# Kernel tuning notes

Hardware: AMD Instinct MI355X
Metric: run time of the kernel (lower is better)

Reference implementation:

```python
import jax, jax.numpy as jnp
import numpy as np

B, C, H, W = 8, 32, 120, 160
MAX_ITER = 3
DAMP = 1e-4
OCC_THRES = 0.1

def setup_inputs():
    key = jax.random.key(0)
    ks = jax.random.split(key, 7)
    R = jnp.broadcast_to(jnp.eye(3, dtype=jnp.float32), (B, 3, 3))
    t = 0.01 * jax.random.normal(ks[0], (B, 3), jnp.float32)
    F0 = jax.random.normal(ks[1], (B, C, H, W), jnp.float32)
    F1 = jax.random.normal(ks[2], (B, C, H, W), jnp.float32)
    invD0 = 0.1 + 0.9 * jax.random.uniform(ks[3], (B, 1, H, W), dtype=jnp.float32)
    invD1 = 0.1 + 0.9 * jax.random.uniform(ks[4], (B, 1, H, W), dtype=jnp.float32)
    K = jnp.broadcast_to(jnp.array([150.0, 150.0, (W - 1) / 2.0, (H - 1) / 2.0], jnp.float32), (B, 4))
    sigma0 = jax.random.uniform(ks[5], (B, 1, H, W), dtype=jnp.float32)
    sigma1 = jax.random.uniform(ks[6], (B, 1, H, W), dtype=jnp.float32)
    return {"R": R, "t": t, "F0": F0, "F1": F1, "invD0": invD0, "invD1": invD1,
            "K": K, "sigma0": sigma0, "sigma1": sigma1}

def _sobel_grad(F):
    # Sobel gradient with replicate padding, normalized (feature_gradient)
    b, c, h, w = F.shape
    kx = jnp.array([[-1., 0., 1.], [-2., 0., 2.], [-1., 0., 1.]], F.dtype).reshape(1, 1, 3, 3)
    ky = jnp.array([[-1., -2., -1.], [0., 0., 0.], [1., 2., 1.]], F.dtype).reshape(1, 1, 3, 3)
    Fp = jnp.pad(F.reshape(b * c, 1, h, w), ((0, 0), (0, 0), (1, 1), (1, 1)), mode='edge')
    dn = ('NCHW', 'OIHW', 'NCHW')
    dx = jax.lax.conv_general_dilated(Fp, kx, (1, 1), 'VALID', dimension_numbers=dn)
    dy = jax.lax.conv_general_dilated(Fp, ky, (1, 1), 'VALID', dimension_numbers=dn)
    mag = jnp.sqrt(dx * dx + dy * dy + 1e-8)
    return (dx / mag).reshape(b, c, h, w), (dy / mag).reshape(b, c, h, w)

def _warp_features(F, u, v):
    # bilinear sampling of F [B,C,H,W] at pixel coords u, v [B,1,H,W], border clamp
    b, c, h, w = F.shape
    u = jnp.clip(u.reshape(b, -1), 0.0, w - 1.0)
    v = jnp.clip(v.reshape(b, -1), 0.0, h - 1.0)
    x0 = jnp.floor(u); y0 = jnp.floor(v)
    wx = (u - x0)[:, None, :]; wy = (v - y0)[:, None, :]
    x0i = x0.astype(jnp.int32); y0i = y0.astype(jnp.int32)
    x1i = jnp.minimum(x0i + 1, w - 1); y1i = jnp.minimum(y0i + 1, h - 1)
    Ff = F.reshape(b, c, h * w)
    def g(yi, xi):
        idx = jnp.broadcast_to((yi * w + xi)[:, None, :], (b, c, yi.shape[-1]))
        return jnp.take_along_axis(Ff, idx, axis=2)
    out = (g(y0i, x0i) * (1 - wx) * (1 - wy) + g(y0i, x1i) * wx * (1 - wy)
           + g(y1i, x0i) * (1 - wx) * wy + g(y1i, x1i) * wx * wy)
    return out.reshape(b, c, h, w)

def _xy_grid(K, b, h, w):
    fx, fy, cx, cy = K[:, 0], K[:, 1], K[:, 2], K[:, 3]
    uu, vv = jnp.meshgrid(jnp.arange(w, dtype=K.dtype), jnp.arange(h, dtype=K.dtype))
    px = (uu[None] - cx[:, None, None]) / fx[:, None, None]
    py = (vv[None] - cy[:, None, None]) / fy[:, None, None]
    return px[:, None], py[:, None]  # [B,1,H,W]

def _warp_inverse_depth(px, py, invD, Rm, t, K):
    b, _, h, w = px.shape
    xyz = jnp.concatenate([px, py, jnp.ones_like(px)], axis=1).reshape(b, 3, h * w)
    warped = jnp.matmul(Rm, xyz) + t[:, :, None] * invD.reshape(b, 1, h * w)
    x_, y_, s_ = warped[:, 0], warped[:, 1], warped[:, 2]
    fx, fy, cx, cy = K[:, 0:1], K[:, 1:2], K[:, 2:3], K[:, 3:4]
    u = (x_ / s_) * fx + cx
    v = (y_ / s_) * fy + cy
    inv_z = invD.reshape(b, h * w) / s_
    return u.reshape(b, 1, h, w), v.reshape(b, 1, h, w), inv_z.reshape(b, 1, h, w)

def _jacobian_warping(invD, K, px, py, Rm, t):
    # compute_Jacobian_warping with pose: returns dx_dp, dy_dp each [B,HW,6]
    b, _, h, w = invD.shape
    xyz = jnp.concatenate([px, py, invD], axis=1).reshape(b, 3, h * w)
    warped = jnp.matmul(Rm, xyz) + t[:, :, None]
    x = warped[:, 0][..., None]; y = warped[:, 1][..., None]; iz = warped[:, 2][..., None]
    xy = x * y
    o = jnp.zeros_like(x)
    dx_dp = jnp.concatenate([-xy, 1 + x * x, -y, iz, o, -iz * x], axis=2)
    dy_dp = jnp.concatenate([-1 - y * y, xy, x, o, iz, -iz * y], axis=2)
    fx = K[:, 0].reshape(b, 1, 1); fy = K[:, 1].reshape(b, 1, 1)
    return dx_dp * fx, dy_dp * fy

def _se3_exp(xi):
    # xi [B,6] = [omega(3), v(3)] matching Jacobian column order (rotation first)
    w = xi[:, :3]; v = xi[:, 3:]
    th2 = jnp.sum(w * w, axis=1, keepdims=True)
    th = jnp.sqrt(th2 + 1e-12)
    a = jnp.sin(th) / th
    bb = (1 - jnp.cos(th)) / (th2 + 1e-12)
    cc = (1 - a) / (th2 + 1e-12)
    z = jnp.zeros_like(w[:, 0])
    wx = jnp.stack([z, -w[:, 2], w[:, 1],
                    w[:, 2], z, -w[:, 0],
                    -w[:, 1], w[:, 0], z], axis=1).reshape(-1, 3, 3)
    wx2 = jnp.matmul(wx, wx)
    I = jnp.eye(3, dtype=xi.dtype)[None]
    Rm = I + a[..., None] * wx + bb[..., None] * wx2
    V = I + bb[..., None] * wx + cc[..., None] * wx2
    dt = jnp.matmul(V, v[..., None])[..., 0]
    return Rm, dt

def _forward(R, t, F0, F1, invD0, invD1, K, sigma0, sigma1):
    b, c, h, w = F0.shape
    hw = h * w
    px, py = _xy_grid(K, b, h, w)
    # feature gradient of F1 is pose-independent -> hoisted out of the loop
    JF_x, JF_y = _sobel_grad(F1)
    weights = jnp.ones_like(F0)
    for _ in range(MAX_ITER):
        # --- compute_warped_residual ---
        u, v, inv_z = _warp_inverse_depth(px, py, invD0, R, t, K)
        F1w = _warp_features(F1, u, v)
        invD1w = _warp_features(invD1, u, v)
        inview = (u > 0) & (u < w - 1) & (v > 0) & (v < h - 1)
        occ = ~((inv_z > invD1w - OCC_THRES) & inview)  # [B,1,H,W]
        res = jnp.where(occ, jnp.asarray(0.001, F0.dtype), F1w - F0)  # [B,C,H,W]
        # --- compute_Jacobian (J_p = -dF/dp) ---
        JFxw = _warp_features(JF_x, u, v).reshape(b, c, hw, 1)
        JFyw = _warp_features(JF_y, u, v).reshape(b, c, hw, 1)
        Jx_p, Jy_p = _jacobian_warping(invD0, K, px, py, R, t)  # [B,HW,6]
        J_p = -(JFxw * Jx_p[:, None] + JFyw * Jy_p[:, None]).reshape(b, c * hw, 6)
        # --- robust weights (Cauchy m-estimator stand-in for mEst_func) ---
        weights = 1.0 / (1.0 + res * res)
        # --- damped Gauss-Newton solve (directSolver stand-in) ---
        JtWJ = jnp.einsum('bnk,bnl->bkl', J_p, J_p)
        rhs = jnp.einsum('bnk,bn->bk', J_p, (weights * res).reshape(b, -1))
        A = JtWJ + DAMP * jnp.eye(6, dtype=J_p.dtype)[None]
        dp = jnp.linalg.solve(A, rhs[..., None])[..., 0]
        dR, dt = _se3_exp(dp)
        t = jnp.matmul(dR, t[..., None])[..., 0] + dt
        R = jnp.matmul(dR, R)
    # pack pose + weights into one array: [B, 9 + 3 + C*H*W]
    return jnp.concatenate([R.reshape(b, 9), t, weights.reshape(b, -1)], axis=1)

def reference(R, t, F0, F1, invD0, invD1, K, sigma0, sigma1):
    return _forward(R, t, F0, F1, invD0, invD1, K, sigma0, sigma1)
```

## Files before the change

### kernel.cpp

```cpp
#include <hip/hip_runtime.h>
#include <math.h>

#define Bn 8
#define Cn 32
#define Hn 120
#define Wn 160
#define HW (Hn*Wn)
#define CHW (Cn*HW)
#define OUTB (12 + CHW)
#define DAMP_C 1e-4
#define OCC_THRES_C 0.1f

#define NCG 4
#define CPG (Cn/NCG)
#define BPB (HW/256)

__global__ void init_kernel(const float* __restrict__ R_in,
                            const float* __restrict__ t_in,
                            float* __restrict__ pose,
                            float* __restrict__ accum) {
    int b = threadIdx.x;
    if (b < Bn) {
        for (int i = 0; i < 9; ++i) pose[b*12 + i] = R_in[b*9 + i];
        for (int i = 0; i < 3; ++i) pose[b*12 + 9 + i] = t_in[b*3 + i];
        for (int i = 0; i < 32; ++i) accum[b*32 + i] = 0.0f;
    }
}

__global__ __launch_bounds__(256) void sobel_kernel(const float* __restrict__ F1,
                                                    float2* __restrict__ G) {
    int idx = blockIdx.x * 256 + threadIdx.x;
    int p = idx % HW;
    int plane = idx / HW;
    int y = p / Wn, x = p % Wn;
    const float* Fp = F1 + (size_t)plane * HW;
    int ym = max(y-1, 0) * Wn, yc = y * Wn, yp = min(y+1, Hn-1) * Wn;
    int xm = max(x-1, 0), xp = min(x+1, Wn-1);
    float a00 = Fp[ym+xm], a01 = Fp[ym+x], a02 = Fp[ym+xp];
    float a10 = Fp[yc+xm],                 a12 = Fp[yc+xp];
    float a20 = Fp[yp+xm], a21 = Fp[yp+x], a22 = Fp[yp+xp];
    float dx = (a02 - a00) + 2.0f*(a12 - a10) + (a22 - a20);
    float dy = (a20 - a00) + 2.0f*(a21 - a01) + (a22 - a02);
    float mag = sqrtf(dx*dx + dy*dy + 1e-8f);
    G[idx] = make_float2(dx / mag, dy / mag);
}

template<bool LAST>
__global__ __launch_bounds__(256) void accum_kernel(
    const float* __restrict__ F0, const float* __restrict__ F1,
    const float* __restrict__ invD0, const float* __restrict__ invD1,
    const float* __restrict__ Kin,
    const float2* __restrict__ G,
    const float* __restrict__ pose, float* __restrict__ accum,
    float* __restrict__ out)
{
    __shared__ float sp[16];
    __shared__ float sred[4*27];
    int blk = blockIdx.x;
    int pblk = blk % BPB;
    int cg   = (blk / BPB) % NCG;
    int b    = blk / (BPB * NCG);
    int p = pblk * 256 + threadIdx.x;
    if (threadIdx.x < 12) sp[threadIdx.x] = pose[b*12 + threadIdx.x];
    else if (threadIdx.x < 16) sp[threadIdx.x] = Kin[b*4 + threadIdx.x - 12];
    __syncthreads();
    float R0=sp[0],R1=sp[1],R2=sp[2],R3=sp[3],R4=sp[4],R5=sp[5],R6=sp[6],R7=sp[7],R8=sp[8];
    float t0=sp[9],t1=sp[10],t2=sp[11];
    float fx=sp[12],fy=sp[13],cx=sp[14],cy=sp[15];

    int y = p / Wn, x = p % Wn;
    float px = ((float)x - cx) / fx;
    float py = ((float)y - cy) / fy;
    float d = invD0[(size_t)b*HW + p];

    float X = R0*px + R1*py + R2 + t0*d;
    float Y = R3*px + R4*py + R5 + t1*d;
    float S = R6*px + R7*py + R8 + t2*d;
    float u = X / S * fx + cx;
    float v = Y / S * fy + cy;
    float iz = d / S;
    bool inview = (u > 0.0f) && (u < (float)(Wn-1)) && (v > 0.0f) && (v < (float)(Hn-1));

    float uc = fminf(fmaxf(u, 0.0f), (float)(Wn-1));
    float vc = fminf(fmaxf(v, 0.0f), (float)(Hn-1));
    float x0f = floorf(uc), y0f = floorf(vc);
    float wx = uc - x0f, wy = vc - y0f;
    int x0 = (int)x0f, y0 = (int)y0f;
    int x1 = min(x0+1, Wn-1), y1 = min(y0+1, Hn-1);
    int i00 = y0*Wn + x0, i01 = y0*Wn + x1, i10 = y1*Wn + x0, i11 = y1*Wn + x1;
    float w00 = (1.0f-wx)*(1.0f-wy), w01 = wx*(1.0f-wy);
    float w10 = (1.0f-wx)*wy,        w11 = wx*wy;

    const float* iD1 = invD1 + (size_t)b*HW;
    float invD1w = iD1[i00]*w00 + iD1[i01]*w01 + iD1[i10]*w10 + iD1[i11]*w11;
    bool occ = !((iz > invD1w - OCC_THRES_C) && inview);

    float xj  = R0*px + R1*py + R2*d + t0;
    float yj  = R3*px + R4*py + R5*d + t1;
    float izj = R6*px + R7*py + R8*d + t2;
    float Jx[6], Jy[6];
    Jx[0] = -xj*yj*fx;        Jx[1] = (1.0f + xj*xj)*fx; Jx[2] = -yj*fx;
    Jx[3] = izj*fx;           Jx[4] = 0.0f;              Jx[5] = -izj*xj*fx;
    Jy[0] = -(1.0f + yj*yj)*fy; Jy[1] = xj*yj*fy;        Jy[2] = xj*fy;
    Jy[3] = 0.0f;             Jy[4] = izj*fy;            Jy[5] = -izj*yj*fy;

    const float*  F0b = F0 + (size_t)b*CHW + p;
    const float*  F1b = F1 + (size_t)b*CHW;
    const float2* Gb  = G  + (size_t)b*CHW;
    int cbase0 = cg * CPG * HW;
    float A2 = 0.0f, B2 = 0.0f, ABc = 0.0f, Sx = 0.0f, Sy = 0.0f;
    #pragma unroll
    for (int cc = 0; cc < CPG; ++cc) {
        int base = cbase0 + cc * HW;
        float2 g00 = Gb[base+i00], g01 = Gb[base+i01];
        float2 g10 = Gb[base+i10], g11 = Gb[base+i11];
        float f1w = F1b[base+i00]*w00 + F1b[base+i01]*w01 + F1b[base+i10]*w10 + F1b[base+i11]*w11;
        float gx  = g00.x*w00 + g01.x*w01 + g10.x*w10 + g11.x*w11;
        float gy  = g00.y*w00 + g01.y*w01 + g10.y*w10 + g11.y*w11;
        float r = occ ? 0.001f : (f1w - F0b[base]);
        float wt = 1.0f / (1.0f + r*r);
        if (LAST) __builtin_nontemporal_store(wt, &out[(size_t)b*OUTB + 12 + base + p]);
        A2 += gx*gx; B2 += gy*gy; ABc += gx*gy;
        float wr = wt * r;
        Sx += wr*gx; Sy += wr*gy;
    }

    float part[27];
    {
        int idx = 0;
        #pragma unroll
        for (int k = 0; k < 6; ++k)
            #pragma unroll
            for (int l = k; l < 6; ++l)
                part[idx++] = A2*Jx[k]*Jx[l] + ABc*(Jx[k]*Jy[l] + Jy[k]*Jx[l]) + B2*Jy[k]*Jy[l];
        #pragma unroll
        for (int k = 0; k < 6; ++k) part[21+k] = -(Sx*Jx[k] + Sy*Jy[k]);
    }

    #pragma unroll
    for (int i = 0; i < 27; ++i) {
        float vsum = part[i];
        for (int off = 32; off > 0; off >>= 1) vsum += __shfl_down(vsum, off, 64);
        part[i] = vsum;
    }
    int lane = threadIdx.x & 63, wave = threadIdx.x >> 6;
    if (lane == 0)
        for (int i = 0; i < 27; ++i) sred[wave*27 + i] = part[i];
    __syncthreads();
    if (threadIdx.x < 27) {
        float s = sred[threadIdx.x] + sred[27+threadIdx.x] + sred[54+threadIdx.x] + sred[81+threadIdx.x];
        atomicAdd(&accum[b*32 + threadIdx.x], s);
    }
}

__global__ void solve_kernel(float* __restrict__ pose, float* __restrict__ accum,
                             float* __restrict__ out, int write_out) {
    int b = threadIdx.x;
    if (b >= Bn) return;
    double A[6][7];
    {
        float acc[27];
        for (int i = 0; i < 27; ++i) acc[i] = accum[b*32 + i];
        int idx = 0;
        for (int k = 0; k < 6; ++k)
            for (int l = k; l < 6; ++l) {
                double vv = (double)acc[idx++];
                A[k][l] = vv; A[l][k] = vv;
            }
        for (int k = 0; k < 6; ++k) { A[k][k] += DAMP_C; A[k][6] = (double)acc[21+k]; }
        for (int i = 0; i < 32; ++i) accum[b*32 + i] = 0.0f;
    }
    for (int col = 0; col < 6; ++col) {
        int piv = col;
        double mx = fabs(A[col][col]);
        for (int r = col+1; r < 6; ++r) { double a = fabs(A[r][col]); if (a > mx) { mx = a; piv = r; } }
        if (piv != col)
            for (int j = col; j < 7; ++j) { double tmp = A[col][j]; A[col][j] = A[piv][j]; A[piv][j] = tmp; }
        double inv = 1.0 / A[col][col];
        for (int r = col+1; r < 6; ++r) {
            double f = A[r][col] * inv;
            for (int j = col; j < 7; ++j) A[r][j] -= f * A[col][j];
        }
    }
    double dp[6];
    for (int col = 5; col >= 0; --col) {
        double s = A[col][6];
        for (int j = col+1; j < 6; ++j) s -= A[col][j] * dp[j];
        dp[col] = s / A[col][col];
    }
    double w0 = dp[0], w1 = dp[1], w2 = dp[2];
    double v0 = dp[3], v1 = dp[4], v2 = dp[5];
    double th2 = w0*w0 + w1*w1 + w2*w2;
    double th = sqrt(th2 + 1e-12);
    float thf = (float)th;
    double sth = (double)sinf(thf);
    double cth = (double)cosf(thf);
    double a = sth / th;
    double bb = (1.0 - cth) / (th2 + 1e-12);
    double cc = (1.0 - a) / (th2 + 1e-12);
    double wxm[3][3] = {{0,-w2,w1},{w2,0,-w0},{-w1,w0,0}};
    double wx2[3][3];
    for (int i = 0; i < 3; ++i)
        for (int j = 0; j < 3; ++j) {
            double s = 0;
            for (int k = 0; k < 3; ++k) s += wxm[i][k]*wxm[k][j];
            wx2[i][j] = s;
        }
    double dR[3][3], V[3][3];
    for (int i = 0; i < 3; ++i)
        for (int j = 0; j < 3; ++j) {
            double I = (i == j) ? 1.0 : 0.0;
            dR[i][j] = I + a*wxm[i][j] + bb*wx2[i][j];
            V[i][j]  = I + bb*wxm[i][j] + cc*wx2[i][j];
        }
    double dt[3];
    for (int i = 0; i < 3; ++i) dt[i] = V[i][0]*v0 + V[i][1]*v1 + V[i][2]*v2;
    double Ro[3][3], to[3];
    for (int i = 0; i < 9; ++i) Ro[i/3][i%3] = (double)pose[b*12 + i];
    for (int i = 0; i < 3; ++i) to[i] = (double)pose[b*12 + 9 + i];
    double tn[3], Rn[3][3];
    for (int i = 0; i < 3; ++i)
        tn[i] = dR[i][0]*to[0] + dR[i][1]*to[1] + dR[i][2]*to[2] + dt[i];
    for (int i = 0; i < 3; ++i)
        for (int j = 0; j < 3; ++j)
            Rn[i][j] = dR[i][0]*Ro[0][j] + dR[i][1]*Ro[1][j] + dR[i][2]*Ro[2][j];
    for (int i = 0; i < 9; ++i) pose[b*12 + i] = (float)Rn[i/3][i%3];
    for (int i = 0; i < 3; ++i) pose[b*12 + 9 + i] = (float)tn[i];
    if (write_out) {
        for (int i = 0; i < 9; ++i) out[(size_t)b*OUTB + i] = (float)Rn[i/3][i%3];
        for (int i = 0; i < 3; ++i) out[(size_t)b*OUTB + 9 + i] = (float)tn[i];
    }
}

extern "C" void kernel_launch(void* const* d_in, const int* in_sizes, int n_in,
                              void* d_out, int out_size, void* d_ws, size_t ws_size,
                              hipStream_t stream) {
    const float* R_in  = (const float*)d_in[0];
    const float* t_in  = (const float*)d_in[1];
    const float* F0    = (const float*)d_in[2];
    const float* F1    = (const float*)d_in[3];
    const float* invD0 = (const float*)d_in[4];
    const float* invD1 = (const float*)d_in[5];
    const float* Kin   = (const float*)d_in[6];
    float* out = (float*)d_out;

    float2* G    = (float2*)d_ws;
    float* accum = (float*)(G + (size_t)Bn*CHW);
    float* pose  = accum + Bn*32;

    init_kernel<<<1, 64, 0, stream>>>(R_in, t_in, pose, accum);
    sobel_kernel<<<(Bn*CHW)/256, 256, 0, stream>>>(F1, G);

    for (int it = 0; it < 3; ++it) {
        bool last = (it == 2);
        if (last)
            accum_kernel<true><<<Bn*NCG*BPB, 256, 0, stream>>>(
                F0, F1, invD0, invD1, Kin, G, pose, accum, out);
        else
            accum_kernel<false><<<Bn*NCG*BPB, 256, 0, stream>>>(
                F0, F1, invD0, invD1, Kin, G, pose, accum, out);
        solve_kernel<<<1, 64, 0, stream>>>(pose, accum, out, last ? 1 : 0);
    }
}
```

Measured before the change: 250.2 us.

## Store gradients and features in fp16 and batch gather loads per channel group

The prep kernel now writes the Sobel gradients, F1 and F0 as half precision copies, and the accumulation kernel reads these instead of the fp32 tensors. The gather loop is split into two groups of four channels, with all loads issued before the arithmetic to expose memory-level parallelism. This cuts the bytes read in each of the three Gauss-Newton iterations, at the cost of an extra conversion pass over F0 and F1. It also adds fp16 rounding error to the residuals and weights, which may exceed the output tolerance.

```diff
diff --git a/kernel.cpp b/kernel.cpp
--- a/kernel.cpp
+++ b/kernel.cpp
@@ -1,4 +1,5 @@
 #include <hip/hip_runtime.h>
+#include <hip/hip_fp16.h>
 #include <math.h>
 
 #define Bn 8
@@ -27,8 +28,11 @@
     }
 }
 
-__global__ __launch_bounds__(256) void sobel_kernel(const float* __restrict__ F1,
-                                                    float2* __restrict__ G) {
+__global__ __launch_bounds__(256) void prep_kernel(const float* __restrict__ F1,
+                                                   const float* __restrict__ F0,
+                                                   __half2* __restrict__ Gh,
+                                                   __half* __restrict__ F1h,
+                                                   __half* __restrict__ F0h) {
     int idx = blockIdx.x * 256 + threadIdx.x;
     int p = idx % HW;
     int plane = idx / HW;
@@ -37,20 +41,22 @@
     int ym = max(y-1, 0) * Wn, yc = y * Wn, yp = min(y+1, Hn-1) * Wn;
     int xm = max(x-1, 0), xp = min(x+1, Wn-1);
     float a00 = Fp[ym+xm], a01 = Fp[ym+x], a02 = Fp[ym+xp];
-    float a10 = Fp[yc+xm],                 a12 = Fp[yc+xp];
+    float a10 = Fp[yc+xm], a11 = Fp[yc+x], a12 = Fp[yc+xp];
     float a20 = Fp[yp+xm], a21 = Fp[yp+x], a22 = Fp[yp+xp];
     float dx = (a02 - a00) + 2.0f*(a12 - a10) + (a22 - a20);
     float dy = (a20 - a00) + 2.0f*(a21 - a01) + (a22 - a02);
     float mag = sqrtf(dx*dx + dy*dy + 1e-8f);
-    G[idx] = make_float2(dx / mag, dy / mag);
+    Gh[idx]  = __floats2half2_rn(dx / mag, dy / mag);
+    F1h[idx] = __float2half(a11);
+    F0h[idx] = __float2half(F0[idx]);
 }
 
 template<bool LAST>
 __global__ __launch_bounds__(256) void accum_kernel(
-    const float* __restrict__ F0, const float* __restrict__ F1,
     const float* __restrict__ invD0, const float* __restrict__ invD1,
     const float* __restrict__ Kin,
-    const float2* __restrict__ G,
+    const __half* __restrict__ F1h, const __half* __restrict__ F0h,
+    const __half2* __restrict__ Gh,
     const float* __restrict__ pose, float* __restrict__ accum,
     float* __restrict__ out)
 {
@@ -104,25 +110,40 @@
     Jy[0] = -(1.0f + yj*yj)*fy; Jy[1] = xj*yj*fy;        Jy[2] = xj*fy;
     Jy[3] = 0.0f;             Jy[4] = izj*fy;            Jy[5] = -izj*yj*fy;
 
-    const float*  F0b = F0 + (size_t)b*CHW + p;
-    const float*  F1b = F1 + (size_t)b*CHW;
-    const float2* Gb  = G  + (size_t)b*CHW;
+    const __half*  F1b = F1h + (size_t)b*CHW;
+    const __half*  F0b = F0h + (size_t)b*CHW + p;
+    const __half2* Gb  = Gh  + (size_t)b*CHW;
     int cbase0 = cg * CPG * HW;
     float A2 = 0.0f, B2 = 0.0f, ABc = 0.0f, Sx = 0.0f, Sy = 0.0f;
     #pragma unroll
-    for (int cc = 0; cc < CPG; ++cc) {
-        int base = cbase0 + cc * HW;
-        float2 g00 = Gb[base+i00], g01 = Gb[base+i01];
-        float2 g10 = Gb[base+i10], g11 = Gb[base+i11];
-        float f1w = F1b[base+i00]*w00 + F1b[base+i01]*w01 + F1b[base+i10]*w10 + F1b[base+i11]*w11;
-        float gx  = g00.x*w00 + g01.x*w01 + g10.x*w10 + g11.x*w11;
-        float gy  = g00.y*w00 + g01.y*w01 + g10.y*w10 + g11.y*w11;
-        float r = occ ? 0.001f : (f1w - F0b[base]);
-        float wt = 1.0f / (1.0f + r*r);
-        if (LAST) __builtin_nontemporal_store(wt, &out[(size_t)b*OUTB + 12 + base + p]);
-        A2 += gx*gx; B2 += gy*gy; ABc += gx*gy;
-        float wr = wt * r;
-        Sx += wr*gx; Sy += wr*gy;
+    for (int hb = 0; hb < 2; ++hb) {
+        __half  l00[4], l01[4], l10[4], l11[4], lf0[4];
+        __half2 g00[4], g01[4], g10[4], g11[4];
+        #pragma unroll
+        for (int cc = 0; cc < 4; ++cc) {
+            int base = cbase0 + (hb*4 + cc) * HW;
+            l00[cc] = F1b[base+i00]; l01[cc] = F1b[base+i01];
+            l10[cc] = F1b[base+i10]; l11[cc] = F1b[base+i11];
+            g00[cc] = Gb[base+i00];  g01[cc] = Gb[base+i01];
+            g10[cc] = Gb[base+i10];  g11[cc] = Gb[base+i11];
+            lf0[cc] = F0b[base];
+        }
+        #pragma unroll
+        for (int cc = 0; cc < 4; ++cc) {
+            int base = cbase0 + (hb*4 + cc) * HW;
+            float f1w = __half2float(l00[cc])*w00 + __half2float(l01[cc])*w01
+                      + __half2float(l10[cc])*w10 + __half2float(l11[cc])*w11;
+            float2 G00 = __half22float2(g00[cc]), G01 = __half22float2(g01[cc]);
+            float2 G10 = __half22float2(g10[cc]), G11 = __half22float2(g11[cc]);
+            float gx = G00.x*w00 + G01.x*w01 + G10.x*w10 + G11.x*w11;
+            float gy = G00.y*w00 + G01.y*w01 + G10.y*w10 + G11.y*w11;
+            float r = occ ? 0.001f : (f1w - __half2float(lf0[cc]));
+            float wt = 1.0f / (1.0f + r*r);
+            if (LAST) __builtin_nontemporal_store(wt, &out[(size_t)b*OUTB + 12 + base + p]);
+            A2 += gx*gx; B2 += gy*gy; ABc += gx*gy;
+            float wr = wt * r;
+            Sx += wr*gx; Sy += wr*gy;
+        }
     }
 
     float part[27];
@@ -244,21 +265,23 @@
     const float* Kin   = (const float*)d_in[6];
     float* out = (float*)d_out;
 
-    float2* G    = (float2*)d_ws;
-    float* accum = (float*)(G + (size_t)Bn*CHW);
+    __half2* Gh  = (__half2*)d_ws;
+    __half*  F1h = (__half*)(Gh + (size_t)Bn*CHW);
+    __half*  F0h = F1h + (size_t)Bn*CHW;
+    float* accum = (float*)(F0h + (size_t)Bn*CHW);
     float* pose  = accum + Bn*32;
 
     init_kernel<<<1, 64, 0, stream>>>(R_in, t_in, pose, accum);
-    sobel_kernel<<<(Bn*CHW)/256, 256, 0, stream>>>(F1, G);
+    prep_kernel<<<(Bn*CHW)/256, 256, 0, stream>>>(F1, F0, Gh, F1h, F0h);
 
     for (int it = 0; it < 3; ++it) {
         bool last = (it == 2);
         if (last)
             accum_kernel<true><<<Bn*NCG*BPB, 256, 0, stream>>>(
-                F0, F1, invD0, invD1, Kin, G, pose, accum, out);
+                invD0, invD1, Kin, F1h, F0h, Gh, pose, accum, out);
         else
             accum_kernel<false><<<Bn*NCG*BPB, 256, 0, stream>>>(
-                F0, F1, invD0, invD1, Kin, G, pose, accum, out);
+                invD0, invD1, Kin, F1h, F0h, Gh, pose, accum, out);
         solve_kernel<<<1, 64, 0, stream>>>(pose, accum, out, last ? 1 : 0);
     }
 }
```

After: 228.2 us. -8.8%, faster.

## Store features and gradients as channel-last fp16 for vectorized bilinear gathers

Applied to the files above, without the earlier changes.

The prep kernel now writes Sobel gradients, F1 and F0 in a pixel-major, channel-innermost layout using half precision. The accumulation kernel then fetches each channel group's eight values per bilinear corner with a few 16-byte loads instead of many scattered fp32 loads. This cuts gather traffic and the number of memory transactions across the three Gauss-Newton iterations. The cost is fp16 rounding of features and gradients, which changes numerics, plus a strided transposed write pattern in the prep kernel.

```diff
diff --git a/kernel.cpp b/kernel.cpp
--- a/kernel.cpp
+++ b/kernel.cpp
@@ -1,4 +1,5 @@
 #include <hip/hip_runtime.h>
+#include <hip/hip_fp16.h>
 #include <math.h>
 
 #define Bn 8
@@ -15,6 +16,9 @@
 #define CPG (Cn/NCG)
 #define BPB (HW/256)
 
+union H8  { ulonglong2 q;    __half  h[8];  };
+union G8  { ulonglong2 q[2]; __half2 h2[8]; };
+
 __global__ void init_kernel(const float* __restrict__ R_in,
                             const float* __restrict__ t_in,
                             float* __restrict__ pose,
@@ -27,30 +31,37 @@
     }
 }
 
-__global__ __launch_bounds__(256) void sobel_kernel(const float* __restrict__ F1,
-                                                    float2* __restrict__ G) {
+__global__ __launch_bounds__(256) void prep_kernel(const float* __restrict__ F1,
+                                                   const float* __restrict__ F0,
+                                                   __half2* __restrict__ Gt,
+                                                   __half* __restrict__ F1t,
+                                                   __half* __restrict__ F0t) {
     int idx = blockIdx.x * 256 + threadIdx.x;
     int p = idx % HW;
     int plane = idx / HW;
+    int b = plane / Cn, c = plane % Cn;
     int y = p / Wn, x = p % Wn;
     const float* Fp = F1 + (size_t)plane * HW;
     int ym = max(y-1, 0) * Wn, yc = y * Wn, yp = min(y+1, Hn-1) * Wn;
     int xm = max(x-1, 0), xp = min(x+1, Wn-1);
     float a00 = Fp[ym+xm], a01 = Fp[ym+x], a02 = Fp[ym+xp];
-    float a10 = Fp[yc+xm],                 a12 = Fp[yc+xp];
+    float a10 = Fp[yc+xm], a11 = Fp[yc+x], a12 = Fp[yc+xp];
     float a20 = Fp[yp+xm], a21 = Fp[yp+x], a22 = Fp[yp+xp];
     float dx = (a02 - a00) + 2.0f*(a12 - a10) + (a22 - a20);
     float dy = (a20 - a00) + 2.0f*(a21 - a01) + (a22 - a02);
     float mag = sqrtf(dx*dx + dy*dy + 1e-8f);
-    G[idx] = make_float2(dx / mag, dy / mag);
+    size_t tidx = ((size_t)b*HW + p)*Cn + c;
+    Gt[tidx]  = __floats2half2_rn(dx / mag, dy / mag);
+    F1t[tidx] = __float2half(a11);
+    F0t[tidx] = __float2half(F0[idx]);
 }
 
 template<bool LAST>
 __global__ __launch_bounds__(256) void accum_kernel(
-    const float* __restrict__ F0, const float* __restrict__ F1,
     const float* __restrict__ invD0, const float* __restrict__ invD1,
     const float* __restrict__ Kin,
-    const float2* __restrict__ G,
+    const __half* __restrict__ F1t, const __half* __restrict__ F0t,
+    const __half2* __restrict__ Gt,
     const float* __restrict__ pose, float* __restrict__ accum,
     float* __restrict__ out)
 {
@@ -104,22 +115,40 @@
     Jy[0] = -(1.0f + yj*yj)*fy; Jy[1] = xj*yj*fy;        Jy[2] = xj*fy;
     Jy[3] = 0.0f;             Jy[4] = izj*fy;            Jy[5] = -izj*yj*fy;
 
-    const float*  F0b = F0 + (size_t)b*CHW + p;
-    const float*  F1b = F1 + (size_t)b*CHW;
-    const float2* Gb  = G  + (size_t)b*CHW;
-    int cbase0 = cg * CPG * HW;
+    const __half*  F1b = F1t + (size_t)b*HW*Cn;
+    const __half*  F0b = F0t + (size_t)b*HW*Cn;
+    const __half2* Gb  = Gt  + (size_t)b*HW*Cn;
+    int co = cg * CPG;
+    size_t t00 = (size_t)i00*Cn + co, t01 = (size_t)i01*Cn + co;
+    size_t t10 = (size_t)i10*Cn + co, t11 = (size_t)i11*Cn + co;
+    H8 f00, f01, f10, f11, ff0;
+    G8 g00, g01, g10, g11;
+    f00.q = *reinterpret_cast<const ulonglong2*>(F1b + t00);
+    f01.q = *reinterpret_cast<const ulonglong2*>(F1b + t01);
+    f10.q = *reinterpret_cast<const ulonglong2*>(F1b + t10);
+    f11.q = *reinterpret_cast<const ulonglong2*>(F1b + t11);
+    g00.q[0] = *reinterpret_cast<const ulonglong2*>(Gb + t00);
+    g00.q[1] = *reinterpret_cast<const ulonglong2*>(Gb + t00 + 4);
+    g01.q[0] = *reinterpret_cast<const ulonglong2*>(Gb + t01);
+    g01.q[1] = *reinterpret_cast<const ulonglong2*>(Gb + t01 + 4);
+    g10.q[0] = *reinterpret_cast<const ulonglong2*>(Gb + t10);
+    g10.q[1] = *reinterpret_cast<const ulonglong2*>(Gb + t10 + 4);
+    g11.q[0] = *reinterpret_cast<const ulonglong2*>(Gb + t11);
+    g11.q[1] = *reinterpret_cast<const ulonglong2*>(Gb + t11 + 4);
+    ff0.q = *reinterpret_cast<const ulonglong2*>(F0b + (size_t)p*Cn + co);
+
     float A2 = 0.0f, B2 = 0.0f, ABc = 0.0f, Sx = 0.0f, Sy = 0.0f;
     #pragma unroll
     for (int cc = 0; cc < CPG; ++cc) {
-        int base = cbase0 + cc * HW;
-        float2 g00 = Gb[base+i00], g01 = Gb[base+i01];
-        float2 g10 = Gb[base+i10], g11 = Gb[base+i11];
-        float f1w = F1b[base+i00]*w00 + F1b[base+i01]*w01 + F1b[base+i10]*w10 + F1b[base+i11]*w11;
-        float gx  = g00.x*w00 + g01.x*w01 + g10.x*w10 + g11.x*w11;
-        float gy  = g00.y*w00 + g01.y*w01 + g10.y*w10 + g11.y*w11;
-        float r = occ ? 0.001f : (f1w - F0b[base]);
+        float f1w = __half2float(f00.h[cc])*w00 + __half2float(f01.h[cc])*w01
+                  + __half2float(f10.h[cc])*w10 + __half2float(f11.h[cc])*w11;
+        float2 G00 = __half22float2(g00.h2[cc]), G01 = __half22float2(g01.h2[cc]);
+        float2 G10 = __half22float2(g10.h2[cc]), G11 = __half22float2(g11.h2[cc]);
+        float gx = G00.x*w00 + G01.x*w01 + G10.x*w10 + G11.x*w11;
+        float gy = G00.y*w00 + G01.y*w01 + G10.y*w10 + G11.y*w11;
+        float r = occ ? 0.001f : (f1w - __half2float(ff0.h[cc]));
         float wt = 1.0f / (1.0f + r*r);
-        if (LAST) __builtin_nontemporal_store(wt, &out[(size_t)b*OUTB + 12 + base + p]);
+        if (LAST) __builtin_nontemporal_store(wt, &out[(size_t)b*OUTB + 12 + (co+cc)*HW + p]);
         A2 += gx*gx; B2 += gy*gy; ABc += gx*gy;
         float wr = wt * r;
         Sx += wr*gx; Sy += wr*gy;
@@ -244,21 +273,23 @@
     const float* Kin   = (const float*)d_in[6];
     float* out = (float*)d_out;
 
-    float2* G    = (float2*)d_ws;
-    float* accum = (float*)(G + (size_t)Bn*CHW);
+    __half2* Gt  = (__half2*)d_ws;
+    __half*  F1t = (__half*)(Gt + (size_t)Bn*CHW);
+    __half*  F0t = F1t + (size_t)Bn*CHW;
+    float* accum = (float*)(F0t + (size_t)Bn*CHW);
     float* pose  = accum + Bn*32;
 
     init_kernel<<<1, 64, 0, stream>>>(R_in, t_in, pose, accum);
-    sobel_kernel<<<(Bn*CHW)/256, 256, 0, stream>>>(F1, G);
+    prep_kernel<<<(Bn*CHW)/256, 256, 0, stream>>>(F1, F0, Gt, F1t, F0t);
 
     for (int it = 0; it < 3; ++it) {
         bool last = (it == 2);
         if (last)
             accum_kernel<true><<<Bn*NCG*BPB, 256, 0, stream>>>(
-                F0, F1, invD0, invD1, Kin, G, pose, accum, out);
+                invD0, invD1, Kin, F1t, F0t, Gt, pose, accum, out);
         else
             accum_kernel<false><<<Bn*NCG*BPB, 256, 0, stream>>>(
-                F0, F1, invD0, invD1, Kin, G, pose, accum, out);
+                invD0, invD1, Kin, F1t, F0t, Gt, pose, accum, out);
         solve_kernel<<<1, 64, 0, stream>>>(pose, accum, out, last ? 1 : 0);
     }
 }
```

After: 405.5 us. 62.0% more time.

## Store features and gradients as channel-last fp16 for vectorized bilinear gathers

Applied to the files above, without the earlier changes.

Replaces the Sobel kernel with a prep kernel that computes gradients and transposes F0, F1, Gx and Gy into a pixel-major, channel-minor fp16 layout through shared memory. The accumulation kernel then fetches 8 channels per bilinear corner with one 16-byte load, where it previously issued scattered per-channel fp32 loads. This cuts gather traffic and the number of memory transactions across the three iterations. The cost is an extra transpose pass and fp16 rounding of features and gradients, which could shift the residuals, weights and solved pose.

```diff
diff --git a/kernel.cpp b/kernel.cpp
--- a/kernel.cpp
+++ b/kernel.cpp
@@ -1,4 +1,5 @@
 #include <hip/hip_runtime.h>
+#include <hip/hip_fp16.h>
 #include <math.h>
 
 #define Bn 8
@@ -15,6 +16,11 @@
 #define CPG (Cn/NCG)
 #define BPB (HW/256)
 
+#define TPX 64
+#define NTILE (HW/TPX)
+
+union H8 { ulonglong2 q; __half h[8]; };
+
 __global__ void init_kernel(const float* __restrict__ R_in,
                             const float* __restrict__ t_in,
                             float* __restrict__ pose,
@@ -27,30 +33,65 @@
     }
 }
 
-__global__ __launch_bounds__(256) void sobel_kernel(const float* __restrict__ F1,
-                                                    float2* __restrict__ G) {
-    int idx = blockIdx.x * 256 + threadIdx.x;
-    int p = idx % HW;
-    int plane = idx / HW;
+__global__ __launch_bounds__(256) void prep_kernel(
+    const float* __restrict__ F1, const float* __restrict__ F0,
+    __half* __restrict__ F1t, __half* __restrict__ F0t,
+    __half* __restrict__ Gxt, __half* __restrict__ Gyt)
+{
+    __shared__ __align__(16) __half sF1[TPX][40];
+    __shared__ __align__(16) __half sF0[TPX][40];
+    __shared__ __align__(16) __half sGx[TPX][40];
+    __shared__ __align__(16) __half sGy[TPX][40];
+    int tile = blockIdx.x % NTILE;
+    int b    = blockIdx.x / NTILE;
+    int p0 = tile * TPX;
+    int p_in = threadIdx.x & 63;
+    int c0   = threadIdx.x >> 6;
+    int p = p0 + p_in;
     int y = p / Wn, x = p % Wn;
-    const float* Fp = F1 + (size_t)plane * HW;
-    int ym = max(y-1, 0) * Wn, yc = y * Wn, yp = min(y+1, Hn-1) * Wn;
-    int xm = max(x-1, 0), xp = min(x+1, Wn-1);
-    float a00 = Fp[ym+xm], a01 = Fp[ym+x], a02 = Fp[ym+xp];
-    float a10 = Fp[yc+xm],                 a12 = Fp[yc+xp];
-    float a20 = Fp[yp+xm], a21 = Fp[yp+x], a22 = Fp[yp+xp];
-    float dx = (a02 - a00) + 2.0f*(a12 - a10) + (a22 - a20);
-    float dy = (a20 - a00) + 2.0f*(a21 - a01) + (a22 - a02);
-    float mag = sqrtf(dx*dx + dy*dy + 1e-8f);
-    G[idx] = make_float2(dx / mag, dy / mag);
+    int ym = max(y-1,0)*Wn, yc = y*Wn, yp = min(y+1,Hn-1)*Wn;
+    int xm = max(x-1,0), xp = min(x+1,Wn-1);
+    H8 rf1, rf0, rgx, rgy;
+    #pragma unroll
+    for (int k = 0; k < 8; ++k) {
+        int c = c0*8 + k;
+        const float* Fp = F1 + ((size_t)b*Cn + c)*HW;
+        float a00=Fp[ym+xm], a01=Fp[ym+x], a02=Fp[ym+xp];
+        float a10=Fp[yc+xm], a11=Fp[yc+x], a12=Fp[yc+xp];
+        float a20=Fp[yp+xm], a21=Fp[yp+x], a22=Fp[yp+xp];
+        float dx = (a02-a00) + 2.0f*(a12-a10) + (a22-a20);
+        float dy = (a20-a00) + 2.0f*(a21-a01) + (a22-a02);
+        float mag = sqrtf(dx*dx + dy*dy + 1e-8f);
+        rgx.h[k] = __float2half(dx / mag);
+        rgy.h[k] = __float2half(dy / mag);
+        rf1.h[k] = __float2half(a11);
+        rf0.h[k] = __float2half(F0[((size_t)b*Cn + c)*HW + p]);
+    }
+    *reinterpret_cast<ulonglong2*>(&sF1[p_in][c0*8]) = rf1.q;
+    *reinterpret_cast<ulonglong2*>(&sF0[p_in][c0*8]) = rf0.q;
+    *reinterpret_cast<ulonglong2*>(&sGx[p_in][c0*8]) = rgx.q;
+    *reinterpret_cast<ulonglong2*>(&sGy[p_in][c0*8]) = rgy.q;
+    __syncthreads();
+    int cq = threadIdx.x & 3;
+    int pi = threadIdx.x >> 2;
+    H8 of1, of0, ogx, ogy;
+    of1.q = *reinterpret_cast<const ulonglong2*>(&sF1[pi][cq*8]);
+    of0.q = *reinterpret_cast<const ulonglong2*>(&sF0[pi][cq*8]);
+    ogx.q = *reinterpret_cast<const ulonglong2*>(&sGx[pi][cq*8]);
+    ogy.q = *reinterpret_cast<const ulonglong2*>(&sGy[pi][cq*8]);
+    size_t o = ((size_t)b*HW + p0 + pi)*Cn + cq*8;
+    *reinterpret_cast<ulonglong2*>(F1t + o) = of1.q;
+    *reinterpret_cast<ulonglong2*>(F0t + o) = of0.q;
+    *reinterpret_cast<ulonglong2*>(Gxt + o) = ogx.q;
+    *reinterpret_cast<ulonglong2*>(Gyt + o) = ogy.q;
 }
 
 template<bool LAST>
 __global__ __launch_bounds__(256) void accum_kernel(
-    const float* __restrict__ F0, const float* __restrict__ F1,
     const float* __restrict__ invD0, const float* __restrict__ invD1,
     const float* __restrict__ Kin,
-    const float2* __restrict__ G,
+    const __half* __restrict__ F1t, const __half* __restrict__ F0t,
+    const __half* __restrict__ Gxt, const __half* __restrict__ Gyt,
     const float* __restrict__ pose, float* __restrict__ accum,
     float* __restrict__ out)
 {
@@ -104,22 +145,42 @@
     Jy[0] = -(1.0f + yj*yj)*fy; Jy[1] = xj*yj*fy;        Jy[2] = xj*fy;
     Jy[3] = 0.0f;             Jy[4] = izj*fy;            Jy[5] = -izj*yj*fy;
 
-    const float*  F0b = F0 + (size_t)b*CHW + p;
-    const float*  F1b = F1 + (size_t)b*CHW;
-    const float2* Gb  = G  + (size_t)b*CHW;
-    int cbase0 = cg * CPG * HW;
+    const __half* F1b = F1t + (size_t)b*HW*Cn;
+    const __half* F0b = F0t + (size_t)b*HW*Cn;
+    const __half* Gxb = Gxt + (size_t)b*HW*Cn;
+    const __half* Gyb = Gyt + (size_t)b*HW*Cn;
+    int co = cg * CPG;
+    size_t t00 = (size_t)i00*Cn + co, t01 = (size_t)i01*Cn + co;
+    size_t t10 = (size_t)i10*Cn + co, t11 = (size_t)i11*Cn + co;
+    H8 f00, f01, f10, f11, ff0;
+    H8 gx00, gx01, gx10, gx11;
+    H8 gy00, gy01, gy10, gy11;
+    f00.q  = *reinterpret_cast<const ulonglong2*>(F1b + t00);
+    f01.q  = *reinterpret_cast<const ulonglong2*>(F1b + t01);
+    f10.q  = *reinterpret_cast<const ulonglong2*>(F1b + t10);
+    f11.q  = *reinterpret_cast<const ulonglong2*>(F1b + t11);
+    gx00.q = *reinterpret_cast<const ulonglong2*>(Gxb + t00);
+    gx01.q = *reinterpret_cast<const ulonglong2*>(Gxb + t01);
+    gx10.q = *reinterpret_cast<const ulonglong2*>(Gxb + t10);
+    gx11.q = *reinterpret_cast<const ulonglong2*>(Gxb + t11);
+    gy00.q = *reinterpret_cast<const ulonglong2*>(Gyb + t00);
+    gy01.q = *reinterpret_cast<const ulonglong2*>(Gyb + t01);
+    gy10.q = *reinterpret_cast<const ulonglong2*>(Gyb + t10);
+    gy11.q = *reinterpret_cast<const ulonglong2*>(Gyb + t11);
+    ff0.q  = *reinterpret_cast<const ulonglong2*>(F0b + (size_t)p*Cn + co);
+
     float A2 = 0.0f, B2 = 0.0f, ABc = 0.0f, Sx = 0.0f, Sy = 0.0f;
     #pragma unroll
     for (int cc = 0; cc < CPG; ++cc) {
-        int base = cbase0 + cc * HW;
-        float2 g00 = Gb[base+i00], g01 = Gb[base+i01];
-        float2 g10 = Gb[base+i10], g11 = Gb[base+i11];
-        float f1w = F1b[base+i00]*w00 + F1b[base+i01]*w01 + F1b[base+i10]*w10 + F1b[base+i11]*w11;
-        float gx  = g00.x*w00 + g01.x*w01 + g10.x*w10 + g11.x*w11;
-        float gy  = g00.y*w00 + g01.y*w01 + g10.y*w10 + g11.y*w11;
-        float r = occ ? 0.001f : (f1w - F0b[base]);
+        float f1w = __half2float(f00.h[cc])*w00 + __half2float(f01.h[cc])*w01
+                  + __half2float(f10.h[cc])*w10 + __half2float(f11.h[cc])*w11;
+        float gx  = __half2float(gx00.h[cc])*w00 + __half2float(gx01.h[cc])*w01
+                  + __half2float(gx10.h[cc])*w10 + __half2float(gx11.h[cc])*w11;
+        float gy  = __half2float(gy00.h[cc])*w00 + __half2float(gy01.h[cc])*w01
+                  + __half2float(gy10.h[cc])*w10 + __half2float(gy11.h[cc])*w11;
+        float r = occ ? 0.001f : (f1w - __half2float(ff0.h[cc]));
         float wt = 1.0f / (1.0f + r*r);
-        if (LAST) __builtin_nontemporal_store(wt, &out[(size_t)b*OUTB + 12 + base + p]);
+        if (LAST) __builtin_nontemporal_store(wt, &out[(size_t)b*OUTB + 12 + (co+cc)*HW + p]);
         A2 += gx*gx; B2 += gy*gy; ABc += gx*gy;
         float wr = wt * r;
         Sx += wr*gx; Sy += wr*gy;
@@ -244,21 +305,24 @@
     const float* Kin   = (const float*)d_in[6];
     float* out = (float*)d_out;
 
-    float2* G    = (float2*)d_ws;
-    float* accum = (float*)(G + (size_t)Bn*CHW);
+    __half* F1t = (__half*)d_ws;
+    __half* F0t = F1t + (size_t)Bn*CHW;
+    __half* Gxt = F0t + (size_t)Bn*CHW;
+    __half* Gyt = Gxt + (size_t)Bn*CHW;
+    float* accum = (float*)(Gyt + (size_t)Bn*CHW);
     float* pose  = accum + Bn*32;
 
     init_kernel<<<1, 64, 0, stream>>>(R_in, t_in, pose, accum);
-    sobel_kernel<<<(Bn*CHW)/256, 256, 0, stream>>>(F1, G);
+    prep_kernel<<<Bn*NTILE, 256, 0, stream>>>(F1, F0, F1t, F0t, Gxt, Gyt);
 
     for (int it = 0; it < 3; ++it) {
         bool last = (it == 2);
         if (last)
             accum_kernel<true><<<Bn*NCG*BPB, 256, 0, stream>>>(
-                F0, F1, invD0, invD1, Kin, G, pose, accum, out);
+                invD0, invD1, Kin, F1t, F0t, Gxt, Gyt, pose, accum, out);
         else
             accum_kernel<false><<<Bn*NCG*BPB, 256, 0, stream>>>(
-                F0, F1, invD0, invD1, Kin, G, pose, accum, out);
+                invD0, invD1, Kin, F1t, F0t, Gxt, Gyt, pose, accum, out);
         solve_kernel<<<1, 64, 0, stream>>>(pose, accum, out, last ? 1 : 0);
     }
 }
```

Result: slower. 268.1 us (+7.1%).
